# Performance work log

Hardware: AMD Instinct MI355X
Metric: run time of the kernel (lower is better)

The kernel has to match this reference:

```python
import jax, jax.numpy as jnp
import numpy as np

# Module-level constants (GRID_SIZE and anchor count from the original repo's globals)
GH, GW = 52, 52          # GRID_SIZE = [H, W]
A = 9                    # number of anchors
G = GH * GW              # flattened grid cells
L_COOR_OBJ = L_COOR_NOOBJ = L_CONF_OBJ = L_CONF_NOOBJ = 1.0


def setup_inputs() -> dict:
    key = jax.random.key(0)
    k1, k2, k3 = jax.random.split(key, 3)
    pred = jax.random.normal(k1, (256, G, A, 5), dtype=jnp.float32)
    # normalized xywh labels, kept away from the borders so boxes are sane
    label = jax.random.uniform(k2, (256, 4), dtype=jnp.float32, minval=0.05, maxval=0.95)
    anchors = jax.random.uniform(k3, (A, 2), dtype=jnp.float32, minval=0.05, maxval=0.6)
    return {"pred": pred, "label": label, "anchors": anchors}


def _clip_corners(cxy, wh):
    # [N,4] -> clipped (x1,y1,x2,y2), matching the torch max/min with 0/1
    x1 = jnp.maximum(cxy[:, 0] - wh[:, 0] / 2, 0.0)
    y1 = jnp.maximum(cxy[:, 1] - wh[:, 1] / 2, 0.0)
    x2 = jnp.minimum(cxy[:, 0] + wh[:, 0] / 2, 1.0)
    y2 = jnp.minimum(cxy[:, 1] + wh[:, 1] / 2, 1.0)
    return jnp.stack([x1, y1, x2, y2], axis=1)


def _forward(pred_raw, label, anchors):
    B = pred_raw.shape[0]
    flat = jnp.arange(G)
    cx = (flat // GH).astype(jnp.float32)   # x-major flat ordering: flat = x*GH + y
    cy = (flat % GH).astype(jnp.float32)

    # --- YOLOout decode: xy = (sigmoid + cell)/grid, wh = anchors*exp, conf = sigmoid ---
    x = (jax.nn.sigmoid(pred_raw[..., 0]) + cx[None, :, None]) / GW      # [B,G,A]
    y = (jax.nn.sigmoid(pred_raw[..., 1]) + cy[None, :, None]) / GH
    wh = anchors[None, None] * jnp.exp(pred_raw[..., 2:4])               # [B,G,A,2]
    conf = jax.nn.sigmoid(pred_raw[..., 4])                              # [B,G,A]
    pred = jnp.concatenate([x[..., None], y[..., None], wh, conf[..., None]], axis=-1)

    # --- responsible cell / anchor indices ---
    idx_x = jnp.floor(label[:, 0] * GW)
    idx_y = jnp.floor(label[:, 1] * GH)
    idx = (idx_x * GH + idx_y).astype(jnp.int32)                         # [B]
    # NOTE: original uses argmax of squared distance (faithful, even if odd)
    anchor_mask = jnp.argmax(
        jnp.sum((label[:, None, 2:4] - anchors[None]) ** 2, axis=-1), axis=1
    )                                                                    # [B]

    # --- anchors_grid [G,A,4]: cell-center xy + anchor wh ---
    ag_x = jnp.broadcast_to(((cx + 0.5) / GW)[:, None], (G, A))
    ag_y = jnp.broadcast_to(((cy + 0.5) / GH)[:, None], (G, A))
    ag_wh = jnp.broadcast_to(anchors[None], (G, A, 2))
    anchors_grid = jnp.concatenate([ag_x[..., None], ag_y[..., None], ag_wh], axis=-1)

    # --- gather the single responsible prediction per sample ---
    b_idx = jnp.arange(B)
    pred_obj = pred[b_idx, idx, anchor_mask]          # [B,5]
    ag_obj = anchors_grid[idx, anchor_mask]           # [B,4]

    # --- noobj MSE = (sum over all) - (sum over obj entries), static shapes ---
    GA1 = G * A - 1
    coor_sq_all = jnp.sum((pred[..., :4] - anchors_grid[None]) ** 2)
    coor_sq_obj = jnp.sum((pred_obj[:, :4] - ag_obj) ** 2)
    coor_l_noobj = (coor_sq_all - coor_sq_obj) / (B * GA1 * 4)
    conf_l_noobj = (jnp.sum(conf ** 2) - jnp.sum(pred_obj[:, 4] ** 2)) / (B * GA1)

    # --- IoU between gathered obj boxes and labels (argmax over a single box is identity) ---
    label_bb = _clip_corners(label[:, :2], label[:, 2:4])
    pred_bb = _clip_corners(pred_obj[:, :2], pred_obj[:, 2:4])
    ix1 = jnp.maximum(label_bb[:, 0], pred_bb[:, 0])
    iy1 = jnp.maximum(label_bb[:, 1], pred_bb[:, 1])
    ix2 = jnp.minimum(label_bb[:, 2], pred_bb[:, 2])
    iy2 = jnp.minimum(label_bb[:, 3], pred_bb[:, 3])
    # faithful to original: areas computed as x2*y2 (not (x2-x1)*(y2-y1))
    label_area = label_bb[:, 2] * label_bb[:, 3]
    pred_area = pred_bb[:, 2] * pred_bb[:, 3]
    inter_area = jnp.maximum(ix2 - ix1, 0.0) * jnp.maximum(iy2 - iy1, 0.0)
    iou = inter_area / (label_area + pred_area - inter_area)

    coor_l_obj = jnp.mean((pred_obj[:, :4] - label) ** 2)
    conf_l_obj = jnp.mean((pred_obj[:, 4] - iou) ** 2)

    return (coor_l_obj * L_COOR_OBJ + coor_l_noobj * L_COOR_NOOBJ
            + conf_l_obj * L_CONF_OBJ + conf_l_noobj * L_CONF_NOOBJ)


def reference(pred, label, anchors):
    return _forward(pred, label, anchors)
```

## Files before the change

### kernel.cpp

```cpp
#include <hip/hip_runtime.h>


#define GHW     52
#define GCELLS  2704
#define NA      9
#define BATCH   256
#define NBLK    (GCELLS * NA)
#define INV52   (1.0f / 52.0f)
#define NBUCKET 256

#define ELEMS_B 1024
#define NB2     6084
#define Q4_B    1280

typedef const __attribute__((address_space(1))) uint32_t glds_g;
typedef __attribute__((address_space(3))) uint32_t glds_l;

__device__ __forceinline__ float sigmoid_exact(float x) {
    return 1.0f / (1.0f + __expf(-x));
}

__device__ __forceinline__ float sigmoid_fast(float x) {
    return __builtin_amdgcn_rcpf(1.0f + __expf(-x));
}

__device__ __forceinline__ float waveReduceSum(float v) {
#pragma unroll
    for (int o = 32; o > 0; o >>= 1) v += __shfl_down(v, o, 64);
    return v;
}

__global__ __launch_bounds__(256) void yolo_obj_kernel(
        const float* __restrict__ pred,
        const float* __restrict__ label,
        const float* __restrict__ anchors,
        float* __restrict__ ws) {
    __shared__ float anch[18];
    __shared__ float red[4][4];
    int b = threadIdx.x;

    ws[4 + b] = 0.0f;
    ws[4 + NBUCKET + b] = 0.0f;

    if (b < 18) anch[b] = anchors[b];
    __syncthreads();

    float4 lab = ((const float4*)label)[b];
    float lx = lab.x, ly = lab.y, lw = lab.z, lh = lab.w;

    int ix = (int)floorf(lx * 52.0f);
    int iy = (int)floorf(ly * 52.0f);
    int idx = ix * GHW + iy;

    int am = 0; float best = -1.0f;
#pragma unroll
    for (int a = 0; a < NA; ++a) {
        float dw = lw - anch[2 * a];
        float dh = lh - anch[2 * a + 1];
        float d = dw * dw + dh * dh;
        if (d > best) { best = d; am = a; }
    }

    const float* p = pred + (((size_t)b * GCELLS + idx) * NA + am) * 5;
    float v0 = p[0], v1 = p[1], v2 = p[2], v3 = p[3], v4 = p[4];

    float aw = anch[2 * am], ah = anch[2 * am + 1];
    float px = (sigmoid_exact(v0) + (float)ix) * INV52;
    float py = (sigmoid_exact(v1) + (float)iy) * INV52;
    float pw = aw * __expf(v2);
    float ph = ah * __expf(v3);
    float pc = sigmoid_exact(v4);

    float agx = ((float)ix + 0.5f) * INV52;
    float agy = ((float)iy + 0.5f) * INV52;

    float d0 = px - agx, d1 = py - agy, d2 = pw - aw, d3 = ph - ah;
    float coor_sq_obj = d0 * d0 + d1 * d1 + d2 * d2 + d3 * d3;
    float conf_sq_obj = pc * pc;

    float e0 = px - lx, e1 = py - ly, e2 = pw - lw, e3 = ph - lh;
    float coor_obj = e0 * e0 + e1 * e1 + e2 * e2 + e3 * e3;

    float lx1 = fmaxf(lx - lw * 0.5f, 0.0f), ly1 = fmaxf(ly - lh * 0.5f, 0.0f);
    float lx2 = fminf(lx + lw * 0.5f, 1.0f), ly2 = fminf(ly + lh * 0.5f, 1.0f);
    float qx1 = fmaxf(px - pw * 0.5f, 0.0f), qy1 = fmaxf(py - ph * 0.5f, 0.0f);
    float qx2 = fminf(px + pw * 0.5f, 1.0f), qy2 = fminf(py + ph * 0.5f, 1.0f);
    float ix1 = fmaxf(lx1, qx1), iy1 = fmaxf(ly1, qy1);
    float ix2 = fminf(lx2, qx2), iy2 = fminf(ly2, qy2);
    float la = lx2 * ly2, pa = qx2 * qy2;
    float inter = fmaxf(ix2 - ix1, 0.0f) * fmaxf(iy2 - iy1, 0.0f);
    float iou = inter / (la + pa - inter);
    float dcf = pc - iou;
    float conf_obj = dcf * dcf;

    float r0 = waveReduceSum(coor_sq_obj);
    float r1 = waveReduceSum(conf_sq_obj);
    float r2 = waveReduceSum(coor_obj);
    float r3 = waveReduceSum(conf_obj);
    int lane = threadIdx.x & 63, wid = threadIdx.x >> 6;
    if (lane == 0) {
        red[0][wid] = r0; red[1][wid] = r1; red[2][wid] = r2; red[3][wid] = r3;
    }
    __syncthreads();
    if (threadIdx.x < 4) {
        ws[threadIdx.x] = red[threadIdx.x][0] + red[threadIdx.x][1]
                        + red[threadIdx.x][2] + red[threadIdx.x][3];
    }
}

__global__ __launch_bounds__(256) void yolo_noobj_kernel(
        const float* __restrict__ pred,
        const float* __restrict__ anchors,
        float* __restrict__ ws) {
    __shared__ float4 sh4[Q4_B];
    __shared__ float anch[18];
    __shared__ float red[2][4];
    int t = threadIdx.x;

    const float4* __restrict__ g4 = (const float4*)pred;
    size_t f0 = (size_t)blockIdx.x * Q4_B;
    int wbase = t & ~63;

#pragma unroll
    for (int i = 0; i < 5; ++i) {
        __builtin_amdgcn_global_load_lds(
            (glds_g*)(g4 + f0 + i * 256 + t),
            (glds_l*)(sh4 + i * 256 + wbase),
            16, 0, 0);
    }
    if (t < 18) anch[t] = anchors[t];
    __syncthreads();

    const float* sh = (const float*)sh4;
    float coorAcc = 0.0f, confAcc = 0.0f;
#pragma unroll
    for (int h = 0; h < 4; ++h) {
        int le = t + h * 256;
        int e  = blockIdx.x * ELEMS_B + le;
        int a  = e % NA;
        float aw = anch[2 * a], ah = anch[2 * a + 1];

        const float* m = sh + 5 * le;
        float v0 = m[0], v1 = m[1], v2 = m[2], v3 = m[3], v4 = m[4];

        float s0 = sigmoid_fast(v0);
        float s1 = sigmoid_fast(v1);
        float s4 = sigmoid_fast(v4);
        float t0 = (s0 - 0.5f) * INV52;
        float t1 = (s1 - 0.5f) * INV52;
        float t2 = aw * (__expf(v2) - 1.0f);
        float t3 = ah * (__expf(v3) - 1.0f);

        coorAcc += t0 * t0 + t1 * t1 + t2 * t2 + t3 * t3;
        confAcc += s4 * s4;
    }

    float rc = waveReduceSum(coorAcc);
    float rf = waveReduceSum(confAcc);
    int lane = t & 63, wid = t >> 6;
    if (lane == 0) { red[0][wid] = rc; red[1][wid] = rf; }
    __syncthreads();
    if (t == 0) {
        float cs = red[0][0] + red[0][1] + red[0][2] + red[0][3];
        float fs = red[1][0] + red[1][1] + red[1][2] + red[1][3];
        int bk = blockIdx.x & (NBUCKET - 1);
        atomicAdd(&ws[4 + bk], cs);
        atomicAdd(&ws[4 + NBUCKET + bk], fs);
    }
}

__global__ __launch_bounds__(256) void yolo_fin_kernel(
        const float* __restrict__ ws,
        float* __restrict__ out) {
    __shared__ float red[2][4];
    int t = threadIdx.x;
    float c = ws[4 + t];
    float f = ws[4 + NBUCKET + t];
    float rc = waveReduceSum(c);
    float rf = waveReduceSum(f);
    int lane = t & 63, wid = t >> 6;
    if (lane == 0) { red[0][wid] = rc; red[1][wid] = rf; }
    __syncthreads();
    if (t == 0) {
        float coor_all = red[0][0] + red[0][1] + red[0][2] + red[0][3];
        float conf_all = red[1][0] + red[1][1] + red[1][2] + red[1][3];
        float coor_l_noobj = (coor_all - ws[0]) / (float)(BATCH * (NBLK - 1) * 4);
        float conf_l_noobj = (conf_all - ws[1]) / (float)(BATCH * (NBLK - 1));
        float coor_l_obj = ws[2] / (float)(BATCH * 4);
        float conf_l_obj = ws[3] / (float)BATCH;
        out[0] = coor_l_obj + coor_l_noobj + conf_l_obj + conf_l_noobj;
    }
}

extern "C" void kernel_launch(void* const* d_in, const int* in_sizes, int n_in,
                              void* d_out, int out_size, void* d_ws, size_t ws_size,
                              hipStream_t stream) {
    const float* pred    = (const float*)d_in[0];
    const float* label   = (const float*)d_in[1];
    const float* anchors = (const float*)d_in[2];
    float* out = (float*)d_out;
    float* ws  = (float*)d_ws;

    yolo_obj_kernel<<<1, 256, 0, stream>>>(pred, label, anchors, ws);
    yolo_noobj_kernel<<<NB2, 256, 0, stream>>>(pred, anchors, ws);
    yolo_fin_kernel<<<1, 256, 0, stream>>>(ws, out);
}
```

Baseline: 183.8 us.

## Fuse obj kernel into finalizer and replace atomics with per-block partials

Drops the single-block obj kernel launch and moves its work into the final reduction kernel, so the pipeline uses two launches instead of three. The bulk noobj kernel now writes a per-block float2 partial instead of doing bucketed atomicAdds, and the finalizer sums all 6084 partials. Anchor indices are now stepped incrementally instead of taking a modulo per element, and the 1/52 scaling is hoisted out of the loop. The cost is a larger serial reduction in a single-block finalizer, plus a small change in floating-point summation order.

```diff
diff --git a/kernel.cpp b/kernel.cpp
--- a/kernel.cpp
+++ b/kernel.cpp
@@ -7,7 +7,6 @@
 #define BATCH   256
 #define NBLK    (GCELLS * NA)
 #define INV52   (1.0f / 52.0f)
-#define NBUCKET 256
 
 #define ELEMS_B 1024
 #define NB2     6084
@@ -30,22 +29,84 @@
     return v;
 }
 
-__global__ __launch_bounds__(256) void yolo_obj_kernel(
+__global__ __launch_bounds__(256) void yolo_noobj_kernel(
+        const float* __restrict__ pred,
+        const float* __restrict__ anchors,
+        float* __restrict__ ws) {
+    __shared__ float4 sh4[Q4_B];
+    __shared__ float anch[18];
+    __shared__ float red[2][4];
+    int t = threadIdx.x;
+
+    const float4* __restrict__ g4 = (const float4*)pred;
+    size_t f0 = (size_t)blockIdx.x * Q4_B;
+    int wbase = t & ~63;
+
+#pragma unroll
+    for (int i = 0; i < 5; ++i) {
+        __builtin_amdgcn_global_load_lds(
+            (glds_g*)(g4 + f0 + i * 256 + t),
+            (glds_l*)(sh4 + i * 256 + wbase),
+            16, 0, 0);
+    }
+    if (t < 18) anch[t] = anchors[t];
+    __syncthreads();
+
+    const float* sh = (const float*)sh4;
+    unsigned e0 = (unsigned)blockIdx.x * ELEMS_B + (unsigned)t;
+    unsigned a  = e0 % 9u;
+    float accXY = 0.0f, accWH = 0.0f, confAcc = 0.0f;
+#pragma unroll
+    for (int h = 0; h < 4; ++h) {
+        int le = t + h * 256;
+        float aw = anch[2 * a], ah = anch[2 * a + 1];
+
+        const float* m = sh + 5 * le;
+        float v0 = m[0], v1 = m[1], v2 = m[2], v3 = m[3], v4 = m[4];
+
+        float s0 = sigmoid_fast(v0);
+        float s1 = sigmoid_fast(v1);
+        float s4 = sigmoid_fast(v4);
+        float t0 = s0 - 0.5f;
+        float t1 = s1 - 0.5f;
+        float t2 = aw * (__expf(v2) - 1.0f);
+        float t3 = ah * (__expf(v3) - 1.0f);
+
+        accXY  += t0 * t0 + t1 * t1;
+        accWH  += t2 * t2 + t3 * t3;
+        confAcc += s4 * s4;
+
+        a += 4u;
+        if (a >= 9u) a -= 9u;
+    }
+    float coorAcc = accXY * (INV52 * INV52) + accWH;
+
+    float rc = waveReduceSum(coorAcc);
+    float rf = waveReduceSum(confAcc);
+    int lane = t & 63, wid = t >> 6;
+    if (lane == 0) { red[0][wid] = rc; red[1][wid] = rf; }
+    __syncthreads();
+    if (t == 0) {
+        float cs = red[0][0] + red[0][1] + red[0][2] + red[0][3];
+        float fs = red[1][0] + red[1][1] + red[1][2] + red[1][3];
+        ((float2*)(ws + 16))[blockIdx.x] = make_float2(cs, fs);
+    }
+}
+
+__global__ __launch_bounds__(256) void yolo_fin_kernel(
         const float* __restrict__ pred,
         const float* __restrict__ label,
         const float* __restrict__ anchors,
-        float* __restrict__ ws) {
+        const float* __restrict__ ws,
+        float* __restrict__ out) {
     __shared__ float anch[18];
     __shared__ float red[4][4];
-    int b = threadIdx.x;
-
-    ws[4 + b] = 0.0f;
-    ws[4 + NBUCKET + b] = 0.0f;
-
-    if (b < 18) anch[b] = anchors[b];
-    __syncthreads();
-
-    float4 lab = ((const float4*)label)[b];
+    __shared__ float objs[4];
+    int t = threadIdx.x;
+    if (t < 18) anch[t] = anchors[t];
+    __syncthreads();
+
+    float4 lab = ((const float4*)label)[t];
     float lx = lab.x, ly = lab.y, lw = lab.z, lh = lab.w;
 
     int ix = (int)floorf(lx * 52.0f);
@@ -61,7 +122,7 @@
         if (d > best) { best = d; am = a; }
     }
 
-    const float* p = pred + (((size_t)b * GCELLS + idx) * NA + am) * 5;
+    const float* p = pred + (((size_t)t * GCELLS + idx) * NA + am) * 5;
     float v0 = p[0], v1 = p[1], v2 = p[2], v3 = p[3], v4 = p[4];
 
     float aw = anch[2 * am], ah = anch[2 * am + 1];
@@ -93,101 +154,41 @@
     float dcf = pc - iou;
     float conf_obj = dcf * dcf;
 
-    float r0 = waveReduceSum(coor_sq_obj);
-    float r1 = waveReduceSum(conf_sq_obj);
-    float r2 = waveReduceSum(coor_obj);
-    float r3 = waveReduceSum(conf_obj);
-    int lane = threadIdx.x & 63, wid = threadIdx.x >> 6;
-    if (lane == 0) {
-        red[0][wid] = r0; red[1][wid] = r1; red[2][wid] = r2; red[3][wid] = r3;
-    }
-    __syncthreads();
-    if (threadIdx.x < 4) {
-        ws[threadIdx.x] = red[threadIdx.x][0] + red[threadIdx.x][1]
-                        + red[threadIdx.x][2] + red[threadIdx.x][3];
-    }
-}
-
-__global__ __launch_bounds__(256) void yolo_noobj_kernel(
-        const float* __restrict__ pred,
-        const float* __restrict__ anchors,
-        float* __restrict__ ws) {
-    __shared__ float4 sh4[Q4_B];
-    __shared__ float anch[18];
-    __shared__ float red[2][4];
-    int t = threadIdx.x;
-
-    const float4* __restrict__ g4 = (const float4*)pred;
-    size_t f0 = (size_t)blockIdx.x * Q4_B;
-    int wbase = t & ~63;
-
-#pragma unroll
-    for (int i = 0; i < 5; ++i) {
-        __builtin_amdgcn_global_load_lds(
-            (glds_g*)(g4 + f0 + i * 256 + t),
-            (glds_l*)(sh4 + i * 256 + wbase),
-            16, 0, 0);
-    }
-    if (t < 18) anch[t] = anchors[t];
-    __syncthreads();
-
-    const float* sh = (const float*)sh4;
-    float coorAcc = 0.0f, confAcc = 0.0f;
-#pragma unroll
-    for (int h = 0; h < 4; ++h) {
-        int le = t + h * 256;
-        int e  = blockIdx.x * ELEMS_B + le;
-        int a  = e % NA;
-        float aw = anch[2 * a], ah = anch[2 * a + 1];
-
-        const float* m = sh + 5 * le;
-        float v0 = m[0], v1 = m[1], v2 = m[2], v3 = m[3], v4 = m[4];
-
-        float s0 = sigmoid_fast(v0);
-        float s1 = sigmoid_fast(v1);
-        float s4 = sigmoid_fast(v4);
-        float t0 = (s0 - 0.5f) * INV52;
-        float t1 = (s1 - 0.5f) * INV52;
-        float t2 = aw * (__expf(v2) - 1.0f);
-        float t3 = ah * (__expf(v3) - 1.0f);
-
-        coorAcc += t0 * t0 + t1 * t1 + t2 * t2 + t3 * t3;
-        confAcc += s4 * s4;
-    }
-
-    float rc = waveReduceSum(coorAcc);
-    float rf = waveReduceSum(confAcc);
-    int lane = t & 63, wid = t >> 6;
-    if (lane == 0) { red[0][wid] = rc; red[1][wid] = rf; }
-    __syncthreads();
-    if (t == 0) {
-        float cs = red[0][0] + red[0][1] + red[0][2] + red[0][3];
-        float fs = red[1][0] + red[1][1] + red[1][2] + red[1][3];
-        int bk = blockIdx.x & (NBUCKET - 1);
-        atomicAdd(&ws[4 + bk], cs);
-        atomicAdd(&ws[4 + NBUCKET + bk], fs);
-    }
-}
-
-__global__ __launch_bounds__(256) void yolo_fin_kernel(
-        const float* __restrict__ ws,
-        float* __restrict__ out) {
-    __shared__ float red[2][4];
-    int t = threadIdx.x;
-    float c = ws[4 + t];
-    float f = ws[4 + NBUCKET + t];
-    float rc = waveReduceSum(c);
-    float rf = waveReduceSum(f);
+    {
+        float r0 = waveReduceSum(coor_sq_obj);
+        float r1 = waveReduceSum(conf_sq_obj);
+        float r2 = waveReduceSum(coor_obj);
+        float r3 = waveReduceSum(conf_obj);
+        int lane = t & 63, wid = t >> 6;
+        if (lane == 0) {
+            red[0][wid] = r0; red[1][wid] = r1; red[2][wid] = r2; red[3][wid] = r3;
+        }
+        __syncthreads();
+        if (t < 4) {
+            objs[t] = red[t][0] + red[t][1] + red[t][2] + red[t][3];
+        }
+        __syncthreads();
+    }
+
+    const float2* __restrict__ part = (const float2*)(ws + 16);
+    float cAcc = 0.0f, fAcc = 0.0f;
+    for (int k = t; k < NB2; k += 256) {
+        float2 pr = part[k];
+        cAcc += pr.x;
+        fAcc += pr.y;
+    }
+    float rc = waveReduceSum(cAcc);
+    float rf = waveReduceSum(fAcc);
     int lane = t & 63, wid = t >> 6;
     if (lane == 0) { red[0][wid] = rc; red[1][wid] = rf; }
     __syncthreads();
     if (t == 0) {
         float coor_all = red[0][0] + red[0][1] + red[0][2] + red[0][3];
         float conf_all = red[1][0] + red[1][1] + red[1][2] + red[1][3];
-        float coor_l_noobj = (coor_all - ws[0]) / (float)(BATCH * (NBLK - 1) * 4);
-        float conf_l_noobj = (conf_all - ws[1]) / (float)(BATCH * (NBLK - 1));
-        float coor_l_obj = ws[2] / (float)(BATCH * 4);
-        float conf_l_obj = ws[3] / (float)BATCH;
+        float coor_l_noobj = (coor_all - objs[0]) / (float)(BATCH * (NBLK - 1) * 4);
+        float conf_l_noobj = (conf_all - objs[1]) / (float)(BATCH * (NBLK - 1));
+        float coor_l_obj = objs[2] / (float)(BATCH * 4);
+        float conf_l_obj = objs[3] / (float)BATCH;
         out[0] = coor_l_obj + coor_l_noobj + conf_l_obj + conf_l_noobj;
     }
 }
@@ -201,7 +202,6 @@
     float* out = (float*)d_out;
     float* ws  = (float*)d_ws;
 
-    yolo_obj_kernel<<<1, 256, 0, stream>>>(pred, label, anchors, ws);
     yolo_noobj_kernel<<<NB2, 256, 0, stream>>>(pred, anchors, ws);
-    yolo_fin_kernel<<<1, 256, 0, stream>>>(ws, out);
-}
+    yolo_fin_kernel<<<1, 256, 0, stream>>>(pred, label, anchors, ws, out);
+}
```

Result: no change. 186.3 us (+1.4%).
